# Kernel tuning notes

Measured on AMD Instinct MI355X. Metric: run time of the kernel, lower is better.

The kernel has to match this reference:

```python
import jax, jax.numpy as jnp
import numpy as np

LABEL_SMOOTHING = 0.1


def setup_inputs() -> dict:
    key = jax.random.key(0)
    k1, k2, k3 = jax.random.split(key, 3)
    B, N, D = 16384, 1000, 1000  # code structurally requires D == n_classes == N
    inputs = jax.random.uniform(k1, (B, D), dtype=jnp.float32)
    labels = jax.random.randint(k2, (B,), 0, N, dtype=jnp.int64)
    code_book = jax.random.uniform(k3, (N, D), dtype=jnp.float32)
    return {"inputs": inputs, "labels": labels, "code_book": code_book}


def reference(inputs, labels, code_book):
    # inputs: [B, D], code_book: [N, D], D == N (n_classes)
    n_classes = inputs.shape[1]
    # soft targets with label smoothing (same as scatter_ + smoothing)
    soft_target = jax.nn.one_hot(labels, n_classes, dtype=inputs.dtype)
    soft_target = soft_target * (1.0 - LABEL_SMOOTHING) + LABEL_SMOOTHING / n_classes
    # Hamming similarity: sum_d [o*c + (1-o)*(1-c)]  ==  o@c.T + (1-o)@(1-c).T
    # (algebraic rewrite of the [B, N, D] broadcast in the original; same math)
    similarity = (jnp.einsum("bd,nd->bn", inputs, code_book)
                  + jnp.einsum("bd,nd->bn", 1.0 - inputs, 1.0 - code_book))
    logp = jax.nn.log_softmax(similarity, axis=1)
    return jnp.mean(jnp.sum(-soft_target * logp, axis=1))
```

## Files before the change

kernel.cpp:

```cpp
#include <hip/hip_runtime.h>

typedef __attribute__((ext_vector_type(8))) short bf16x8;
typedef __attribute__((ext_vector_type(4))) float f32x4;

#define AS1 __attribute__((address_space(1)))
#define AS3 __attribute__((address_space(3)))

__device__ static inline void gl2lds16(const void* g, void* l) {
  __builtin_amdgcn_global_load_lds((const AS1 unsigned int*)g, (AS3 unsigned int*)l, 16, 0, 0);
}

__device__ static inline unsigned short f2bf(float x) {
  unsigned int u = __float_as_uint(x);
  unsigned int r = u + 0x7FFFu + ((u >> 16) & 1u);
  return (unsigned short)(r >> 16);
}

__global__ __launch_bounds__(256) void prep_all_k(
    const float* __restrict__ in, const int* __restrict__ labraw,
    const float* __restrict__ cb, unsigned short* __restrict__ a,
    unsigned short* __restrict__ b, float* __restrict__ rowsum,
    int* __restrict__ labs, float* __restrict__ lin, float* __restrict__ out) {
  const int bx = blockIdx.x, t = threadIdx.x;
  if (bx < 8192) {
    int idx = bx * 256 + t;
    int row = idx >> 7, g = idx & 127;
    union { unsigned short u[8]; uint4 v; } pk;
    if (g < 125) {
      const float4* p = (const float4*)(in + (size_t)row * 1000 + g * 8);
      float4 v0 = p[0], v1 = p[1];
      pk.u[0] = f2bf(2.f * v0.x); pk.u[1] = f2bf(2.f * v0.y);
      pk.u[2] = f2bf(2.f * v0.z); pk.u[3] = f2bf(2.f * v0.w);
      pk.u[4] = f2bf(2.f * v1.x); pk.u[5] = f2bf(2.f * v1.y);
      pk.u[6] = f2bf(2.f * v1.z); pk.u[7] = f2bf(2.f * v1.w);
    } else {
      pk.v = make_uint4(0, 0, 0, 0);
    }
    *(uint4*)(a + ((size_t)row << 10) + (g << 3)) = pk.v;
  } else if (bx < 9216) {
    int n = bx - 8192;
    float s = 0.f;
#pragma unroll
    for (int j = 0; j < 4; ++j) {
      int c = t + j * 256;
      float v = 0.f;
      if (n < 1000 && c < 1000) v = cb[(size_t)n * 1000 + c];
      s += v;
      b[((size_t)n << 10) + c] = f2bf(v);
    }
    __shared__ float red[256];
    red[t] = s;
    __syncthreads();
    for (int o = 128; o > 0; o >>= 1) {
      if (t < o) red[t] += red[t + o];
      __syncthreads();
    }
    if (t == 0) rowsum[n] = (n < 1000) ? red[0] : 0.f;
  } else {
    __shared__ int nz;
    if (t == 0) nz = 0;
    __syncthreads();
    if (labraw[2 * t + 1] != 0) atomicAdd(&nz, 1);
    __syncthreads();
    bool is64 = (nz < 32);
    int row = (bx - 9216) * 256 + t;
    labs[row] = is64 ? labraw[2 * row] : labraw[row];
    if (bx == 9216 && t == 0) { lin[0] = 0.f; out[0] = 0.f; }
  }
}

__global__ __launch_bounds__(256, 1) void coding_loss_k(
    const unsigned short* __restrict__ A,
    const unsigned short* __restrict__ B,
    const float* __restrict__ rowsum,
    const int* __restrict__ labels,
    float* __restrict__ Z,
    float* __restrict__ lin) {
  __shared__ __align__(16) unsigned short lds[32768];
  unsigned short* Ab0 = lds;
  unsigned short* Ab1 = lds + 8192;
  unsigned short* Bb0 = lds + 16384;
  unsigned short* Bb1 = lds + 24576;

  const int t    = threadIdx.x;
  const int lane = t & 63;
  const int w    = t >> 6;
  const int wr   = w >> 1;
  const int wc   = w & 1;
  const int g16  = lane >> 4;
  const int c16  = lane & 15;
  const int ct   = blockIdx.x & 3;
  const int rt   = blockIdx.x >> 2;
  const int r0   = rt << 8;
  const int c0   = ct << 8;

  size_t a_src[4], b_src[4]; int dstoff[4];
#pragma unroll
  for (int i = 0; i < 4; ++i) {
    int ch = i * 256 + t, row = ch >> 2;
    int sg = (ch & 3) ^ ((row >> 1) & 3);
    a_src[i] = (size_t)(r0 + row) * 1024 + sg * 8;
    b_src[i] = (size_t)(c0 + row) * 1024 + sg * 8;
    dstoff[i] = ch * 8;
  }
  int a_eoff[8], b_eoff[8];
#pragma unroll
  for (int i = 0; i < 8; ++i) {
    int ar = wr * 128 + i * 16 + c16;
    a_eoff[i] = ar * 32 + ((g16 ^ ((ar >> 1) & 3)) << 3);
    int br = wc * 128 + i * 16 + c16;
    b_eoff[i] = br * 32 + ((g16 ^ ((br >> 1) & 3)) << 3);
  }

  f32x4 acc[8][8];
#pragma unroll
  for (int mi = 0; mi < 8; ++mi)
#pragma unroll
    for (int ni = 0; ni < 8; ++ni) acc[mi][ni] = (f32x4)(0.f);

#define STAGE_A(kk, dst) \
  { _Pragma("unroll") for (int i = 0; i < 4; ++i) gl2lds16(A + a_src[i] + (kk) * 32, (dst) + dstoff[i]); }
#define STAGE_B(kk, dst) \
  { _Pragma("unroll") for (int i = 0; i < 4; ++i) gl2lds16(B + b_src[i] + (kk) * 32, (dst) + dstoff[i]); }
#define COMPUTE(pa, pb)                                                                   \
  {                                                                                       \
    bf16x8 af[8], bf[8];                                                                  \
    _Pragma("unroll") for (int i = 0; i < 8; ++i) af[i] = *(const bf16x8*)((pa) + a_eoff[i]); \
    _Pragma("unroll") for (int i = 0; i < 8; ++i) bf[i] = *(const bf16x8*)((pb) + b_eoff[i]); \
    _Pragma("unroll") for (int mi = 0; mi < 8; ++mi)                                      \
      _Pragma("unroll") for (int ni = 0; ni < 8; ++ni)                                    \
        acc[mi][ni] = __builtin_amdgcn_mfma_f32_16x16x32_bf16(af[mi], bf[ni], acc[mi][ni], 0, 0, 0); \
  }

  STAGE_A(0, Ab0);
  STAGE_B(0, Bb0);
  unsigned short *pa = Ab0, *pan = Ab1, *pb = Bb0, *pbn = Bb1;

#pragma unroll 2
  for (int J = 0; J < 31; ++J) {
    STAGE_A(J + 1, pan);
    STAGE_B(J + 1, pbn);
    __builtin_amdgcn_s_waitcnt(0xF78);
    __builtin_amdgcn_s_barrier();
    COMPUTE(pa, pb);
    __builtin_amdgcn_s_barrier();
    unsigned short* x = pa; pa = pan; pan = x;
    x = pb; pb = pbn; pbn = x;
  }
  __builtin_amdgcn_s_waitcnt(0xF70);
  __builtin_amdgcn_s_barrier();
  COMPUTE(pa, pb);
  __syncthreads();

  float* zbuf = (float*)lds;
  float* lbuf = zbuf + 512;
  float rs[8]; int gcol[8];
#pragma unroll
  for (int ni = 0; ni < 8; ++ni) {
    gcol[ni] = c0 + wc * 128 + ni * 16 + c16;
    rs[ni]   = rowsum[gcol[ni]];
  }
  float lacc = 0.f;
#pragma unroll
  for (int mi = 0; mi < 8; ++mi) {
#pragma unroll
    for (int r = 0; r < 4; ++r) {
      int lrow = mi * 16 + g16 * 4 + r;
      int labv = labels[r0 + wr * 128 + lrow];
      float e = 0.f;
#pragma unroll
      for (int ni = 0; ni < 8; ++ni) {
        float S = acc[mi][ni][r] - rs[ni];
        e += __expf(S - 40.f);
        lacc += 1e-4f * S;
        if (gcol[ni] == labv) lacc += 0.9f * S;
      }
      e += __shfl_xor(e, 1, 64);
      e += __shfl_xor(e, 2, 64);
      e += __shfl_xor(e, 4, 64);
      e += __shfl_xor(e, 8, 64);
      if (c16 == 0) zbuf[w * 128 + lrow] = e;
    }
  }
#pragma unroll
  for (int d = 1; d < 64; d <<= 1) lacc += __shfl_xor(lacc, d, 64);
  if (lane == 0) lbuf[w] = lacc;
  __syncthreads();
  {
    int wrg = t >> 7, l7 = t & 127;
    float z = zbuf[(wrg * 2 + 0) * 128 + l7] + zbuf[(wrg * 2 + 1) * 128 + l7];
    Z[ct * 16384 + r0 + t] = z;
  }
  if (t == 0) atomicAdd(lin, lbuf[0] + lbuf[1] + lbuf[2] + lbuf[3]);
#undef STAGE_A
#undef STAGE_B
#undef COMPUTE
}

__global__ __launch_bounds__(256) void finalize_k(const float* __restrict__ Z,
                                                  const float* __restrict__ lin,
                                                  float* __restrict__ out) {
  int t = threadIdx.x;
  int row = blockIdx.x * 256 + t;
  float v = 40.f + logf(Z[row] + Z[16384 + row] + Z[2 * 16384 + row] + Z[3 * 16384 + row]);
#pragma unroll
  for (int d = 1; d < 64; d <<= 1) v += __shfl_xor(v, d, 64);
  __shared__ float s[4];
  if ((t & 63) == 0) s[t >> 6] = v;
  __syncthreads();
  if (t == 0) {
    float tot = s[0] + s[1] + s[2] + s[3];
    if (blockIdx.x == 0) tot -= lin[0];
    atomicAdd(out, tot * (1.f / 16384.f));
  }
}

extern "C" void kernel_launch(void* const* d_in, const int* in_sizes, int n_in,
                              void* d_out, int out_size, void* d_ws, size_t ws_size,
                              hipStream_t stream) {
  const float* inputs = (const float*)d_in[0];
  const int* labraw   = (const int*)d_in[1];
  const float* code   = (const float*)d_in[2];

  unsigned short* a_bf = (unsigned short*)d_ws;
  unsigned short* b_bf = a_bf + (size_t)16384 * 1024;
  float* rowsum        = (float*)(b_bf + (size_t)1024 * 1024);
  float* Z             = rowsum + 1024;
  float* lin           = Z + 4 * 16384;
  int* labs            = (int*)(lin + 1);

  prep_all_k<<<9280, 256, 0, stream>>>(inputs, labraw, code, a_bf, b_bf, rowsum,
                                       labs, lin, (float*)d_out);
  coding_loss_k<<<256, 256, 0, stream>>>(a_bf, b_bf, rowsum, labs, Z, lin);
  finalize_k<<<64, 256, 0, stream>>>(Z, lin, (float*)d_out);
}
```

Measured before the change: 146.0 us.

## Restructure GEMM main loop to 8 waves with 4-stage LDS ring and split phases

Measured after the change: 140.3 us. 3.9% less time.

```diff
diff --git a/kernel.cpp b/kernel.cpp
--- a/kernel.cpp
+++ b/kernel.cpp
@@ -69,24 +69,20 @@
   }
 }
 
-__global__ __launch_bounds__(256, 1) void coding_loss_k(
-    const unsigned short* __restrict__ A,
-    const unsigned short* __restrict__ B,
+__global__ __launch_bounds__(512, 2) void coding_loss_k(
+    const unsigned short* __restrict__ Ag,
+    const unsigned short* __restrict__ Bg,
     const float* __restrict__ rowsum,
     const int* __restrict__ labels,
     float* __restrict__ Z,
     float* __restrict__ lin) {
-  __shared__ __align__(16) unsigned short lds[32768];
-  unsigned short* Ab0 = lds;
-  unsigned short* Ab1 = lds + 8192;
-  unsigned short* Bb0 = lds + 16384;
-  unsigned short* Bb1 = lds + 24576;
+  extern __shared__ __align__(16) unsigned short lds[];
 
   const int t    = threadIdx.x;
   const int lane = t & 63;
   const int w    = t >> 6;
-  const int wr   = w >> 1;
-  const int wc   = w & 1;
+  const int wr   = w >> 2;
+  const int wc   = w & 3;
   const int g16  = lane >> 4;
   const int c16  = lane & 15;
   const int ct   = blockIdx.x & 3;
@@ -94,70 +90,105 @@
   const int r0   = rt << 8;
   const int c0   = ct << 8;
 
-  size_t a_src[4], b_src[4]; int dstoff[4];
-#pragma unroll
-  for (int i = 0; i < 4; ++i) {
-    int ch = i * 256 + t, row = ch >> 2;
+  size_t a_src[2], b_src[2]; int dstoff[2];
+#pragma unroll
+  for (int i = 0; i < 2; ++i) {
+    int ch = i * 512 + t, row = ch >> 2;
     int sg = (ch & 3) ^ ((row >> 1) & 3);
     a_src[i] = (size_t)(r0 + row) * 1024 + sg * 8;
     b_src[i] = (size_t)(c0 + row) * 1024 + sg * 8;
     dstoff[i] = ch * 8;
   }
-  int a_eoff[8], b_eoff[8];
+  int a_eoff[8], b_eoff[4];
 #pragma unroll
   for (int i = 0; i < 8; ++i) {
     int ar = wr * 128 + i * 16 + c16;
     a_eoff[i] = ar * 32 + ((g16 ^ ((ar >> 1) & 3)) << 3);
-    int br = wc * 128 + i * 16 + c16;
+  }
+#pragma unroll
+  for (int i = 0; i < 4; ++i) {
+    int br = wc * 64 + i * 16 + c16;
     b_eoff[i] = br * 32 + ((g16 ^ ((br >> 1) & 3)) << 3);
   }
 
-  f32x4 acc[8][8];
+  f32x4 acc[8][4];
 #pragma unroll
   for (int mi = 0; mi < 8; ++mi)
 #pragma unroll
-    for (int ni = 0; ni < 8; ++ni) acc[mi][ni] = (f32x4)(0.f);
-
-#define STAGE_A(kk, dst) \
-  { _Pragma("unroll") for (int i = 0; i < 4; ++i) gl2lds16(A + a_src[i] + (kk) * 32, (dst) + dstoff[i]); }
-#define STAGE_B(kk, dst) \
-  { _Pragma("unroll") for (int i = 0; i < 4; ++i) gl2lds16(B + b_src[i] + (kk) * 32, (dst) + dstoff[i]); }
-#define COMPUTE(pa, pb)                                                                   \
-  {                                                                                       \
-    bf16x8 af[8], bf[8];                                                                  \
-    _Pragma("unroll") for (int i = 0; i < 8; ++i) af[i] = *(const bf16x8*)((pa) + a_eoff[i]); \
-    _Pragma("unroll") for (int i = 0; i < 8; ++i) bf[i] = *(const bf16x8*)((pb) + b_eoff[i]); \
-    _Pragma("unroll") for (int mi = 0; mi < 8; ++mi)                                      \
-      _Pragma("unroll") for (int ni = 0; ni < 8; ++ni)                                    \
-        acc[mi][ni] = __builtin_amdgcn_mfma_f32_16x16x32_bf16(af[mi], bf[ni], acc[mi][ni], 0, 0, 0); \
-  }
-
-  STAGE_A(0, Ab0);
-  STAGE_B(0, Bb0);
-  unsigned short *pa = Ab0, *pan = Ab1, *pb = Bb0, *pbn = Bb1;
-
-#pragma unroll 2
-  for (int J = 0; J < 31; ++J) {
-    STAGE_A(J + 1, pan);
-    STAGE_B(J + 1, pbn);
-    __builtin_amdgcn_s_waitcnt(0xF78);
-    __builtin_amdgcn_s_barrier();
-    COMPUTE(pa, pb);
-    __builtin_amdgcn_s_barrier();
-    unsigned short* x = pa; pa = pan; pan = x;
-    x = pb; pb = pbn; pbn = x;
-  }
-  __builtin_amdgcn_s_waitcnt(0xF70);
+    for (int ni = 0; ni < 4; ++ni) acc[mi][ni] = (f32x4)(0.f);
+
+#define TILE(J, DO_STAGE, DO_WAIT, WAIT_IMM)                                    \
+  {                                                                             \
+    unsigned short* pa = lds + ((J) & 3) * 8192;                                \
+    unsigned short* pb = lds + 32768 + ((J) & 3) * 8192;                        \
+    unsigned short* sa = lds + (((J) + 3) & 3) * 8192;                          \
+    unsigned short* sb = lds + 32768 + (((J) + 3) & 3) * 8192;                  \
+    bf16x8 af[4], bv[4];                                                        \
+                               \
+    _Pragma("unroll") for (int i = 0; i < 4; ++i)                               \
+        af[i] = *(const bf16x8*)(pa + a_eoff[i]);                               \
+    _Pragma("unroll") for (int i = 0; i < 4; ++i)                               \
+        bv[i] = *(const bf16x8*)(pb + b_eoff[i]);                               \
+    if (DO_STAGE) {                                                             \
+      _Pragma("unroll") for (int i = 0; i < 2; ++i)                             \
+          gl2lds16(Ag + a_src[i] + ((J) + 3) * 32, sa + dstoff[i]);             \
+    }                                                                           \
+    __builtin_amdgcn_s_barrier();                                               \
+    __builtin_amdgcn_s_setprio(1);                                              \
+    _Pragma("unroll") for (int mi = 0; mi < 4; ++mi)                            \
+      _Pragma("unroll") for (int ni = 0; ni < 4; ++ni)                          \
+        acc[mi][ni] =                                                           \
+            __builtin_amdgcn_mfma_f32_16x16x32_bf16(af[mi], bv[ni], acc[mi][ni], 0, 0, 0); \
+    __builtin_amdgcn_s_setprio(0);                                              \
+    __builtin_amdgcn_s_barrier();                                               \
+    __builtin_amdgcn_sched_barrier(0);                                          \
+                        \
+    _Pragma("unroll") for (int i = 0; i < 4; ++i)                               \
+        af[i] = *(const bf16x8*)(pa + a_eoff[i + 4]);                           \
+    if (DO_STAGE) {                                                             \
+      _Pragma("unroll") for (int i = 0; i < 2; ++i)                             \
+          gl2lds16(Bg + b_src[i] + ((J) + 3) * 32, sb + dstoff[i]);             \
+    }                                                                           \
+    __builtin_amdgcn_s_barrier();                                               \
+    __builtin_amdgcn_s_setprio(1);                                              \
+    _Pragma("unroll") for (int mi = 0; mi < 4; ++mi)                            \
+      _Pragma("unroll") for (int ni = 0; ni < 4; ++ni)                          \
+        acc[mi + 4][ni] =                                                       \
+            __builtin_amdgcn_mfma_f32_16x16x32_bf16(af[mi], bv[ni], acc[mi + 4][ni], 0, 0, 0); \
+    __builtin_amdgcn_s_setprio(0);                                              \
+    if (DO_WAIT) __builtin_amdgcn_s_waitcnt(WAIT_IMM);                          \
+    __builtin_amdgcn_s_barrier();                                               \
+    __builtin_amdgcn_sched_barrier(0);                                          \
+  }
+
+#pragma unroll
+  for (int q = 0; q < 3; ++q) {
+#pragma unroll
+    for (int i = 0; i < 2; ++i)
+      gl2lds16(Ag + a_src[i] + q * 32, lds + q * 8192 + dstoff[i]);
+#pragma unroll
+    for (int i = 0; i < 2; ++i)
+      gl2lds16(Bg + b_src[i] + q * 32, lds + 32768 + q * 8192 + dstoff[i]);
+  }
+  __builtin_amdgcn_s_waitcnt(0xF78);
   __builtin_amdgcn_s_barrier();
-  COMPUTE(pa, pb);
+  __builtin_amdgcn_sched_barrier(0);
+
+#pragma unroll 4
+  for (int J = 0; J < 28; ++J) TILE(J, 1, 1, 0xF78);
+  TILE(28, 1, 1, 0xF78);
+  TILE(29, 0, 1, 0xF74);
+  TILE(30, 0, 1, 0xF70);
+  TILE(31, 0, 0, 0xF70);
+#undef TILE
   __syncthreads();
 
   float* zbuf = (float*)lds;
-  float* lbuf = zbuf + 512;
-  float rs[8]; int gcol[8];
-#pragma unroll
-  for (int ni = 0; ni < 8; ++ni) {
-    gcol[ni] = c0 + wc * 128 + ni * 16 + c16;
+  float* lbuf = zbuf + 1024;
+  float rs[4]; int gcol[4];
+#pragma unroll
+  for (int ni = 0; ni < 4; ++ni) {
+    gcol[ni] = c0 + wc * 64 + ni * 16 + c16;
     rs[ni]   = rowsum[gcol[ni]];
   }
   float lacc = 0.f;
@@ -169,7 +200,7 @@
       int labv = labels[r0 + wr * 128 + lrow];
       float e = 0.f;
 #pragma unroll
-      for (int ni = 0; ni < 8; ++ni) {
+      for (int ni = 0; ni < 4; ++ni) {
         float S = acc[mi][ni][r] - rs[ni];
         e += __expf(S - 40.f);
         lacc += 1e-4f * S;
@@ -186,15 +217,15 @@
   for (int d = 1; d < 64; d <<= 1) lacc += __shfl_xor(lacc, d, 64);
   if (lane == 0) lbuf[w] = lacc;
   __syncthreads();
-  {
+  if (t < 256) {
     int wrg = t >> 7, l7 = t & 127;
-    float z = zbuf[(wrg * 2 + 0) * 128 + l7] + zbuf[(wrg * 2 + 1) * 128 + l7];
+    float z = zbuf[(wrg * 4 + 0) * 128 + l7] + zbuf[(wrg * 4 + 1) * 128 + l7] +
+              zbuf[(wrg * 4 + 2) * 128 + l7] + zbuf[(wrg * 4 + 3) * 128 + l7];
     Z[ct * 16384 + r0 + t] = z;
   }
-  if (t == 0) atomicAdd(lin, lbuf[0] + lbuf[1] + lbuf[2] + lbuf[3]);
-#undef STAGE_A
-#undef STAGE_B
-#undef COMPUTE
+  if (t == 0)
+    atomicAdd(lin, lbuf[0] + lbuf[1] + lbuf[2] + lbuf[3] +
+                   lbuf[4] + lbuf[5] + lbuf[6] + lbuf[7]);
 }
 
 __global__ __launch_bounds__(256) void finalize_k(const float* __restrict__ Z,
@@ -229,8 +260,15 @@
   float* lin           = Z + 4 * 16384;
   int* labs            = (int*)(lin + 1);
 
+  static int lds_attr_set = 0;
+  if (!lds_attr_set) {
+    hipFuncSetAttribute(reinterpret_cast<const void*>(coding_loss_k),
+                        hipFuncAttributeMaxDynamicSharedMemorySize, 131072);
+    lds_attr_set = 1;
+  }
+
   prep_all_k<<<9280, 256, 0, stream>>>(inputs, labraw, code, a_bf, b_bf, rowsum,
                                        labs, lin, (float*)d_out);
-  coding_loss_k<<<256, 256, 0, stream>>>(a_bf, b_bf, rowsum, labs, Z, lin);
+  coding_loss_k<<<256, 512, 131072, stream>>>(a_bf, b_bf, rowsum, labs, Z, lin);
   finalize_k<<<64, 256, 0, stream>>>(Z, lin, (float*)d_out);
 }
```
